# Performance work log

Measured on AMD Instinct MI355X. Metric: run time of the kernel, lower is better.

## Reference

```python
import jax, jax.numpy as jnp
import numpy as np

N, E, D = 50000, 800000, 64  # nodes, edges, hidden (in_hid == out_hid, n_heads == 1)


def setup_inputs() -> dict:
    key = jax.random.key(0)
    ks = jax.random.split(key, 12)

    def lin(k, out_d, in_d):
        k1, k2 = jax.random.split(k)
        s = 1.0 / np.sqrt(in_d)
        W = jax.random.uniform(k1, (out_d, in_d), minval=-s, maxval=s, dtype=jnp.float32)
        b = jax.random.uniform(k2, (out_d,), minval=-s, maxval=s, dtype=jnp.float32)
        return W, b

    Wt, bt = lin(ks[0], D, D + 1)   # w_transfer: Linear(d_input+1, d_k)
    Wq, bq = lin(ks[1], D, D)
    Wks, bks = lin(ks[2], D, D)
    Wkd, bkd = lin(ks[3], D, D)
    Wvs, bvs = lin(ks[4], D, D)
    Wvd, bvd = lin(ks[5], D, D)
    return {
        "x": jax.random.normal(ks[6], (N, D), dtype=jnp.float32),
        "edge_index": jax.random.randint(ks[7], (2, E), 0, N),
        "edge_time": jax.random.uniform(ks[8], (E,), dtype=jnp.float32),
        "x_time": jax.random.uniform(ks[9], (N,), dtype=jnp.float32),
        "edge_same": jax.random.randint(ks[10], (E,), 0, 2).astype(jnp.float32),
        "ln_gamma": jnp.ones((D,), jnp.float32),
        "ln_beta": jnp.zeros((D,), jnp.float32),
        "Wt": Wt, "bt": bt, "Wq": Wq, "bq": bq,
        "Wks": Wks, "bks": bks, "Wkd": Wkd, "bkd": bkd,
        "Wvs": Wvs, "bvs": bvs, "Wvd": Wvd, "bvd": bvd,
    }


def _gelu(x):
    return jax.nn.gelu(x, approximate=False)  # torch F.gelu default (erf)


def _temporal_enc(t):
    # TemporalEncoding: div_term[j] = 1/10000^(2*(j//2)/D); sin on even cols, cos on odd
    j = jnp.arange(D)
    div = 1.0 / jnp.power(jnp.float32(10000.0), (2.0 * (j // 2)).astype(jnp.float32) / D)
    pe = (t.reshape(-1, 1) * 200.0) * div[None, :]  # [E, D]
    return jnp.where((j % 2 == 0)[None, :], jnp.sin(pe), jnp.cos(pe))


def reference(x, edge_index, edge_time, x_time, edge_same, ln_gamma, ln_beta,
              Wt, bt, Wq, bq, Wks, bks, Wkd, bkd, Wvs, bvs, Wvd, bvd):
    residual = x
    # LayerNorm(d_input)
    mu = jnp.mean(x, axis=-1, keepdims=True)
    var = jnp.var(x, axis=-1, keepdims=True)
    xn = (x - mu) / jnp.sqrt(var + 1e-5) * ln_gamma + ln_beta

    src, dst = edge_index[0], edge_index[1]  # x_j = source, x_i = target (PyG default)
    x_j = xn[src]                            # [E, D] gather
    x_i = xn[dst]                            # [E, D] gather
    es = edge_same.reshape(-1, 1)            # [E, 1]

    te = _temporal_enc(edge_time)            # [E, D]
    xt = _gelu(jnp.concatenate([x_j, edge_time.reshape(-1, 1)], axis=1) @ Wt.T + bt) + te

    q = x_i @ Wq.T + bq
    k = es * (xt @ Wks.T + bks) + (1.0 - es) * (xt @ Wkd.T + bkd)
    att = jnp.sum(k * q, axis=-1) / jnp.sqrt(jnp.float32(D))  # [E]

    # PyG-style segment softmax over edges sharing the same receiver
    m = jax.ops.segment_max(att, dst, num_segments=N)
    m = jnp.where(jnp.isfinite(m), m, 0.0)
    ex = jnp.exp(att - m[dst])
    denom = jax.ops.segment_sum(ex, dst, num_segments=N)
    attn = ex / (denom[dst] + 1e-16)         # [E]

    v = es * (xt @ Wvs.T + bvs) + (1.0 - es) * (xt @ Wvd.T + bvd)
    aggr = jax.ops.segment_sum(attn[:, None] * v, dst, num_segments=N)  # [N, D]

    return residual + _gelu(aggr)            # dropout is identity in eval
```

## Files before the change

kernel.cpp:

```cpp
#include <hip/hip_runtime.h>
#include <hip/hip_bf16.h>
#include <math.h>

#define D 64

typedef __attribute__((ext_vector_type(8))) short bf16x8;
typedef __attribute__((ext_vector_type(8))) _Float16 f16x8;
typedef __attribute__((ext_vector_type(8))) unsigned short u16x8;
typedef __attribute__((ext_vector_type(4))) float f32x4;
typedef unsigned short u16;

__device__ __forceinline__ float gelu_erf(float x) {
    return 0.5f * x * (1.0f + erff(x * 0.70710678118654752f));
}
__device__ __forceinline__ float gelu_fast(float x) {
    float t = x * fmaf(x * x, -0.1029432f, -2.3022080f);
    float e = __builtin_amdgcn_exp2f(t);
    return x * __builtin_amdgcn_rcpf(1.0f + e);
}
__device__ __forceinline__ u16 f2bf(float v) {
    __hip_bfloat16 h = __float2bfloat16(v);
    return *(u16*)&h;
}
__device__ __forceinline__ float bf2f(u16 v) {
    return __uint_as_float(((unsigned int)v) << 16);
}
__device__ __forceinline__ u16 f2h(float v) {
    _Float16 h = (_Float16)v;
    return __builtin_bit_cast(u16, h);
}
__device__ __forceinline__ void atomic_pk_add_f16(u16* addr, float lo, float hi) {
    unsigned int p = (unsigned int)f2h(lo) | ((unsigned int)f2h(hi) << 16);
    asm volatile("global_atomic_pk_add_f16 %0, %1, off sc1" :: "v"(addr), "v"(p));
}
__device__ __forceinline__ int pi_perm(int p) { return ((p & 3) << 4) | (p >> 2); }

__device__ __forceinline__ float rowsum16(float v) {
    int x;
    x = __builtin_amdgcn_update_dpp(0, __builtin_bit_cast(int, v), 0xB1, 0xF, 0xF, true);
    v += __builtin_bit_cast(float, x);
    x = __builtin_amdgcn_update_dpp(0, __builtin_bit_cast(int, v), 0x4E, 0xF, 0xF, true);
    v += __builtin_bit_cast(float, x);
    x = __builtin_amdgcn_update_dpp(0, __builtin_bit_cast(int, v), 0x141, 0xF, 0xF, true);
    v += __builtin_bit_cast(float, x);
    x = __builtin_amdgcn_update_dpp(0, __builtin_bit_cast(int, v), 0x140, 0xF, 0xF, true);
    v += __builtin_bit_cast(float, x);
    return v;
}

__global__ __launch_bounds__(256) void prep_hist(
    const float* __restrict__ Wt, const float* __restrict__ Wq,
    const float* __restrict__ Wks, const float* __restrict__ Wkd,
    const float* __restrict__ Wvs, const float* __restrict__ Wvd,
    u16* __restrict__ WtB, u16* __restrict__ WqB,
    u16* __restrict__ WksB, u16* __restrict__ WkdB,
    u16* __restrict__ WvsB, u16* __restrict__ WvdB,
    const int* __restrict__ ei, const float* __restrict__ esame,
    int* __restrict__ cnt, int E)
{
    if (blockIdx.x < 12) {
        int task = blockIdx.x * 4 + (threadIdx.x >> 6);
        int lane = threadIdx.x & 63;
        int wsel = task >> 3, f = task & 7;
        int c = lane & 15, quad = lane >> 4;
        int nt = f >> 1, kk = f & 1;
        for (int j = 0; j < 8; ++j) {
            int n = nt * 16 + c, k = kk * 32 + quad * 8 + j;
            float v; u16* dp; bool h16 = false;
            switch (wsel) {
                case 0: v = Wt[n * 65 + k];  dp = WtB;  break;
                case 1: v = Wq[n * 64 + k];  dp = WqB;  break;
                case 2: v = Wks[k * 64 + n]; dp = WksB; break;
                case 3: v = Wkd[k * 64 + n]; dp = WkdB; break;
                case 4: v = Wvs[n * 64 + pi_perm(k)]; dp = WvsB; h16 = true; break;
                default: v = Wvd[n * 64 + pi_perm(k)]; dp = WvdB; h16 = true; break;
            }
            dp[(f * 64 + lane) * 8 + j] = h16 ? f2h(v) : f2bf(v);
        }
    } else {
        int gid = (blockIdx.x - 12) * 256 + threadIdx.x;
        int stride = (gridDim.x - 12) * 256;
        for (int e = gid; e < E; e += stride) {
            int key = 2 * ei[E + e] + (esame[e] > 0.5f ? 0 : 1);
            atomicAdd(&cnt[key], 1);
        }
    }
}

#define SCAN_CHUNK 2048

__global__ __launch_bounds__(256) void scan_phaseA(const int* __restrict__ cnt,
                                                   int* __restrict__ bsum, int M)
{
    int base = blockIdx.x * SCAN_CHUNK;
    int s = 0;
    for (int i = threadIdx.x; i < SCAN_CHUNK; i += 256) {
        int idx = base + i;
        s += (idx < M) ? cnt[idx] : 0;
    }
    #pragma unroll
    for (int o = 32; o; o >>= 1) s += __shfl_xor(s, o);
    __shared__ int red[4];
    if ((threadIdx.x & 63) == 0) red[threadIdx.x >> 6] = s;
    __syncthreads();
    if (threadIdx.x == 0) bsum[blockIdx.x] = red[0] + red[1] + red[2] + red[3];
}

__global__ __launch_bounds__(256) void scan_phaseC(const int* __restrict__ cnt,
                                                   const int* __restrict__ bsum,
                                                   int* __restrict__ cursor, int M)
{
    __shared__ int wsum[4];
    __shared__ int sboff;
    if (threadIdx.x < 64) {
        int v = ((int)threadIdx.x < (int)blockIdx.x) ? bsum[threadIdx.x] : 0;
        #pragma unroll
        for (int o = 32; o; o >>= 1) v += __shfl_xor(v, o);
        if (threadIdx.x == 0) sboff = v;
    }
    int base = blockIdx.x * SCAN_CHUNK;
    int i0 = base + threadIdx.x * 8;
    int vals[8];
    int tsum = 0;
    #pragma unroll
    for (int j = 0; j < 8; ++j) {
        int idx = i0 + j;
        vals[j] = (idx < M) ? cnt[idx] : 0;
        tsum += vals[j];
    }
    int lane = threadIdx.x & 63;
    int w = threadIdx.x >> 6;
    int inc = tsum;
    #pragma unroll
    for (int o = 1; o < 64; o <<= 1) {
        int v = __shfl_up(inc, o);
        if (lane >= o) inc += v;
    }
    if (lane == 63) wsum[w] = inc;
    __syncthreads();
    int woff = 0;
    #pragma unroll
    for (int k = 0; k < 4; ++k) woff += (k < w) ? wsum[k] : 0;
    int excl = woff + (inc - tsum) + sboff;
    #pragma unroll
    for (int j = 0; j < 8; ++j) {
        int idx = i0 + j;
        if (idx < M) cursor[idx] = excl;
        excl += vals[j];
    }
}

__global__ __launch_bounds__(256) void scatter_qgemm(
    const int* __restrict__ ei, const float* __restrict__ et,
    const float* __restrict__ esame, int* __restrict__ cursor,
    int4* __restrict__ evk, int E, int GS,
    const float* __restrict__ x, const float* __restrict__ gamma, const float* __restrict__ beta,
    const u16* __restrict__ WqB, const u16* __restrict__ WksB, const u16* __restrict__ WkdB,
    const float* __restrict__ bq, const float* __restrict__ bks, const float* __restrict__ bkd,
    u16* __restrict__ xnb, u16* __restrict__ qk2, float* __restrict__ bq2, int N)
{
    __shared__ u16 qtile[4][16 * 64];
    __shared__ u16 stile[4][32 * 64];

    if (blockIdx.x < GS) {
        int e = blockIdx.x * 256 + threadIdx.x;
        if (e < E) {
            int key = 2 * ei[E + e] + (esame[e] > 0.5f ? 0 : 1);
            int pos = atomicAdd(&cursor[key], 1);
            evk[pos] = make_int4(key, __float_as_int(et[e]), ei[e], 0);
        }
        return;
    }

    const int lane = threadIdx.x & 63;
    const int c = lane & 15, quad = lane >> 4;
    const int w = threadIdx.x >> 6;
    const int wave = (blockIdx.x - GS) * 4 + w;
    const int n0r = wave * 16;
    const bool active = n0r < N;
    const int n0 = active ? n0r : 0;
    const int rowA = (n0 + c < N) ? n0 + c : N - 1;

    const float* xrow = x + (long)rowA * D;
    f32x4 xa = *(const f32x4*)(xrow + quad * 8);
    f32x4 xb = *(const f32x4*)(xrow + quad * 8 + 4);
    f32x4 xc = *(const f32x4*)(xrow + 32 + quad * 8);
    f32x4 xd = *(const f32x4*)(xrow + 32 + quad * 8 + 4);
    float s = 0.f, s2 = 0.f;
    #pragma unroll
    for (int j = 0; j < 4; ++j) {
        s += xa[j] + xb[j] + xc[j] + xd[j];
        s2 += xa[j] * xa[j] + xb[j] * xb[j] + xc[j] * xc[j] + xd[j] * xd[j];
    }
    s += __shfl_xor(s, 16);  s += __shfl_xor(s, 32);
    s2 += __shfl_xor(s2, 16); s2 += __shfl_xor(s2, 32);
    float mu = s * (1.0f / 64.0f);
    float var = s2 * (1.0f / 64.0f) - mu * mu;
    float rinv = rsqrtf(var + 1e-5f);
    f32x4 ga = *(const f32x4*)(gamma + quad * 8);
    f32x4 gb = *(const f32x4*)(gamma + quad * 8 + 4);
    f32x4 gc = *(const f32x4*)(gamma + 32 + quad * 8);
    f32x4 gd = *(const f32x4*)(gamma + 32 + quad * 8 + 4);
    f32x4 ba = *(const f32x4*)(beta + quad * 8);
    f32x4 bb = *(const f32x4*)(beta + quad * 8 + 4);
    f32x4 bc = *(const f32x4*)(beta + 32 + quad * 8);
    f32x4 bd = *(const f32x4*)(beta + 32 + quad * 8 + 4);
    bf16x8 a0, a1;
    #pragma unroll
    for (int j = 0; j < 4; ++j) {
        a0[j]     = (short)f2bf(fmaf((xa[j] - mu) * rinv, ga[j], ba[j]));
        a0[4 + j] = (short)f2bf(fmaf((xb[j] - mu) * rinv, gb[j], bb[j]));
        a1[j]     = (short)f2bf(fmaf((xc[j] - mu) * rinv, gc[j], bc[j]));
        a1[4 + j] = (short)f2bf(fmaf((xd[j] - mu) * rinv, gd[j], bd[j]));
    }
    *(bf16x8*)(xnb + (long)rowA * D + quad * 8) = a0;
    *(bf16x8*)(xnb + (long)rowA * D + 32 + quad * 8) = a1;

    float bqc[4], bksc[4], bkdc[4];
    #pragma unroll
    for (int t = 0; t < 4; ++t) {
        bqc[t] = bq[t * 16 + c]; bksc[t] = bks[t * 16 + c]; bkdc[t] = bkd[t * 16 + c];
    }

    f32x4 accq[4];
    #pragma unroll
    for (int t = 0; t < 4; ++t) {
        bf16x8 b0 = *(const bf16x8*)(WqB + ((t * 2 + 0) * 64 + lane) * 8);
        bf16x8 b1 = *(const bf16x8*)(WqB + ((t * 2 + 1) * 64 + lane) * 8);
        f32x4 z = {0.f, 0.f, 0.f, 0.f};
        z = __builtin_amdgcn_mfma_f32_16x16x32_bf16(a0, b0, z, 0, 0, 0);
        z = __builtin_amdgcn_mfma_f32_16x16x32_bf16(a1, b1, z, 0, 0, 0);
        accq[t] = z;
    }
    #pragma unroll
    for (int r = 0; r < 4; ++r) {
        float qv[4], ss = 0.f, sd = 0.f;
        #pragma unroll
        for (int t = 0; t < 4; ++t) {
            qv[t] = accq[t][r] + bqc[t];
            ss = fmaf(qv[t], bksc[t], ss);
            sd = fmaf(qv[t], bkdc[t], sd);
        }
        #pragma unroll
        for (int o = 1; o < 16; o <<= 1) { ss += __shfl_xor(ss, o); sd += __shfl_xor(sd, o); }
        int nrow = n0 + quad * 4 + r;
        if (active && c == 0 && nrow < N)
            *(float2*)(bq2 + 2 * nrow) = make_float2(ss, sd);
        #pragma unroll
        for (int t = 0; t < 4; ++t)
            qtile[w][(quad * 4 + r) * 64 + t * 16 + c] = f2bf(qv[t]);
    }
    __syncthreads();

    const u16* qrow = &qtile[w][c * 64 + quad * 8];
    bf16x8 q0 = *(const bf16x8*)(qrow);
    bf16x8 q1 = *(const bf16x8*)(qrow + 32);
    #pragma unroll
    for (int t = 0; t < 4; ++t) {
        bf16x8 bs0 = *(const bf16x8*)(WksB + ((t * 2 + 0) * 64 + lane) * 8);
        bf16x8 bs1 = *(const bf16x8*)(WksB + ((t * 2 + 1) * 64 + lane) * 8);
        bf16x8 bd0 = *(const bf16x8*)(WkdB + ((t * 2 + 0) * 64 + lane) * 8);
        bf16x8 bd1 = *(const bf16x8*)(WkdB + ((t * 2 + 1) * 64 + lane) * 8);
        f32x4 zs = {0.f, 0.f, 0.f, 0.f}, zd = {0.f, 0.f, 0.f, 0.f};
        zs = __builtin_amdgcn_mfma_f32_16x16x32_bf16(q0, bs0, zs, 0, 0, 0);
        zs = __builtin_amdgcn_mfma_f32_16x16x32_bf16(q1, bs1, zs, 0, 0, 0);
        zd = __builtin_amdgcn_mfma_f32_16x16x32_bf16(q0, bd0, zd, 0, 0, 0);
        zd = __builtin_amdgcn_mfma_f32_16x16x32_bf16(q1, bd1, zd, 0, 0, 0);
        #pragma unroll
        for (int r = 0; r < 4; ++r) {
            int m = quad * 4 + r;
            stile[w][(2 * m + 0) * 64 + c * 4 + t] = f2bf(zs[r]);
            stile[w][(2 * m + 1) * 64 + c * 4 + t] = f2bf(zd[r]);
        }
    }
    __syncthreads();
    if (active) {
        int nrows = min(16, N - n0);
        const u16x8* sp = (const u16x8*)&stile[w][0];
        u16x8* dp = (u16x8*)(qk2 + (long)(2 * n0) * D);
        int cnt8 = nrows * 16;
        for (int j = lane; j < cnt8; j += 64) dp[j] = sp[j];
    }
}

template<bool FULL>
__device__ __forceinline__ void edge_run(
    const int4* __restrict__ evk, const u16* __restrict__ xnb,
    const bf16x8* bfrag, const float* btc, const float* w64c,
    const float* dvr, float phr,
    const u16* __restrict__ qk2, const float* __restrict__ bq2,
    u16* __restrict__ A, float* __restrict__ den,
    int base, int end, int qchunk, int c, int quad)
{
    int cur_key = -1;
    float racc0 = 0.f, racc1 = 0.f, racc2 = 0.f, racc3 = 0.f, rden = 0.f;
    float qf0 = 0.f, qf1 = 0.f, qf2 = 0.f, qf3 = 0.f, bqk = 0.f;

    const int rowbase = base + (c >> 2) * qchunk + (c & 3);
    const int qbase   = base + quad * qchunk;

    for (int i = 0; i < qchunk; i += 4) {
        int eidx = rowbase + i;
        int ec = FULL ? eidx : min(eidx, end - 1);
        int srcL = ((const int*)(evk + ec))[2];

        const u16* ar = xnb + srcL * D + quad * 8;
        bf16x8 a0 = *(const bf16x8*)(ar);
        bf16x8 a1 = *(const bf16x8*)(ar + 32);

        int qb = qbase + i;
        int2 kt0 = *(const int2*)(evk + (FULL ? qb     : min(qb,     end - 1)));
        int2 kt1 = *(const int2*)(evk + (FULL ? qb + 1 : min(qb + 1, end - 1)));
        int2 kt2 = *(const int2*)(evk + (FULL ? qb + 2 : min(qb + 2, end - 1)));
        int2 kt3 = *(const int2*)(evk + (FULL ? qb + 3 : min(qb + 3, end - 1)));

        f32x4 acc[4];
        #pragma unroll
        for (int t = 0; t < 4; ++t) {
            f32x4 z = {0.f, 0.f, 0.f, 0.f};
            z = __builtin_amdgcn_mfma_f32_16x16x32_bf16(a0, bfrag[t * 2 + 0], z, 0, 0, 0);
            z = __builtin_amdgcn_mfma_f32_16x16x32_bf16(a1, bfrag[t * 2 + 1], z, 0, 0, 0);
            acc[t] = z;
        }

        #pragma unroll
        for (int r = 0; r < 4; ++r) {
            int2 kt = (r == 0) ? kt0 : (r == 1) ? kt1 : (r == 2) ? kt2 : kt3;
            int keym = kt.x;
            float tm = __int_as_float(kt.y);

            float x0 = acc[0][r] + fmaf(tm, w64c[0], btc[0]);
            float x1 = acc[1][r] + fmaf(tm, w64c[1], btc[1]);
            float x2 = acc[2][r] + fmaf(tm, w64c[2], btc[2]);
            float x3 = acc[3][r] + fmaf(tm, w64c[3], btc[3]);
            float v0 = gelu_fast(x0) + __builtin_amdgcn_sinf(fmaf(tm, dvr[0], phr));
            float v1 = gelu_fast(x1) + __builtin_amdgcn_sinf(fmaf(tm, dvr[1], phr));
            float v2 = gelu_fast(x2) + __builtin_amdgcn_sinf(fmaf(tm, dvr[2], phr));
            float v3 = gelu_fast(x3) + __builtin_amdgcn_sinf(fmaf(tm, dvr[3], phr));

            if (keym != cur_key) {
                if (cur_key >= 0) {
                    u16* ap = A + cur_key * D + c * 4;
                    atomic_pk_add_f16(ap, racc0, racc1);
                    atomic_pk_add_f16(ap + 2, racc2, racc3);
                    if (c == 0) atomicAdd(&den[cur_key], rden);
                }
                cur_key = keym;
                ushort4 q4 = *(const ushort4*)(qk2 + cur_key * D + c * 4);
                qf0 = bf2f(q4.x); qf1 = bf2f(q4.y); qf2 = bf2f(q4.z); qf3 = bf2f(q4.w);
                bqk = bq2[cur_key] * 0.18033688011f;
                racc0 = racc1 = racc2 = racc3 = 0.f;
                rden = 0.f;
            }

            float p = v0 * qf0;
            p = fmaf(v1, qf1, p);
            p = fmaf(v2, qf2, p);
            p = fmaf(v3, qf3, p);
            p = rowsum16(p);

            float ex = __builtin_amdgcn_exp2f(fmaf(p, 0.18033688011f, bqk));
            if (!FULL && (qbase + i + r >= end)) ex = 0.f;

            racc0 = fmaf(ex, v0, racc0);
            racc1 = fmaf(ex, v1, racc1);
            racc2 = fmaf(ex, v2, racc2);
            racc3 = fmaf(ex, v3, racc3);
            rden += ex;
        }
    }

    if (cur_key >= 0) {
        u16* ap = A + cur_key * D + c * 4;
        atomic_pk_add_f16(ap, racc0, racc1);
        atomic_pk_add_f16(ap + 2, racc2, racc3);
        if (c == 0) atomicAdd(&den[cur_key], rden);
    }
}

__global__ __launch_bounds__(256) void edge_pass(
    const int4* __restrict__ evk, const u16* __restrict__ xnb, const u16* __restrict__ WtB,
    const float* __restrict__ Wt, const float* __restrict__ bt,
    const u16* __restrict__ qk2, const float* __restrict__ bq2,
    u16* __restrict__ A, float* __restrict__ den, int E, int chunk)
{
    const int lane = threadIdx.x & 63;
    const int c = lane & 15, quad = lane >> 4;
    const int wave = blockIdx.x * 4 + (threadIdx.x >> 6);
    const int base = wave * chunk;
    if (base >= E) return;
    const int end = min(base + chunk, E);
    const int qchunk = chunk >> 2;

    bf16x8 bfrag[8];
    #pragma unroll
    for (int f = 0; f < 8; ++f)
        bfrag[f] = *(const bf16x8*)(WtB + (f * 64 + lane) * 8);

    float btc[4], w64c[4], dvr[4];
    #pragma unroll
    for (int t = 0; t < 4; ++t) {
        int dim = t * 16 + c;
        btc[t] = bt[dim];
        w64c[t] = Wt[dim * 65 + 64];
        dvr[t] = 31.830988618f * expf(-9.210340371976184f * (float)(2 * (dim >> 1)) * (1.0f / 64.0f));
    }
    const float phr = (c & 1) ? 0.25f : 0.0f;

    if (base + chunk <= E)
        edge_run<true>(evk, xnb, bfrag, btc, w64c, dvr, phr, qk2, bq2, A, den,
                       base, end, qchunk, c, quad);
    else
        edge_run<false>(evk, xnb, bfrag, btc, w64c, dvr, phr, qk2, bq2, A, den,
                        base, end, qchunk, c, quad);
}

__global__ __launch_bounds__(256) void vgemm(
    const float* __restrict__ x, const u16* __restrict__ A, const float* __restrict__ den,
    const u16* __restrict__ WvsB, const u16* __restrict__ WvdB,
    const float* __restrict__ bvs, const float* __restrict__ bvd,
    float* __restrict__ out, int N)
{
    const int lane = threadIdx.x & 63;
    const int c = lane & 15, quad = lane >> 4;
    const int wave = blockIdx.x * 4 + (threadIdx.x >> 6);
    const int n0 = wave * 16;
    if (n0 >= N) return;
    const int rowA = (n0 + c < N) ? n0 + c : N - 1;

    float bvsc[4], bvdc[4];
    #pragma unroll
    for (int t = 0; t < 4; ++t) { bvsc[t] = bvs[t * 16 + c]; bvdc[t] = bvd[t * 16 + c]; }

    const u16* srow = A + (long)(2 * rowA) * D + quad * 8;
    const u16* drow = A + (long)(2 * rowA + 1) * D + quad * 8;
    f16x8 s0 = *(const f16x8*)(srow);
    f16x8 s1 = *(const f16x8*)(srow + 32);
    f16x8 d0 = *(const f16x8*)(drow);
    f16x8 d1 = *(const f16x8*)(drow + 32);

    f32x4 oacc[4];
    #pragma unroll
    for (int t = 0; t < 4; ++t) {
        f16x8 bs0 = *(const f16x8*)(WvsB + ((t * 2 + 0) * 64 + lane) * 8);
        f16x8 bs1 = *(const f16x8*)(WvsB + ((t * 2 + 1) * 64 + lane) * 8);
        f16x8 bd0 = *(const f16x8*)(WvdB + ((t * 2 + 0) * 64 + lane) * 8);
        f16x8 bd1 = *(const f16x8*)(WvdB + ((t * 2 + 1) * 64 + lane) * 8);
        f32x4 z = {0.f, 0.f, 0.f, 0.f};
        z = __builtin_amdgcn_mfma_f32_16x16x32_f16(s0, bs0, z, 0, 0, 0);
        z = __builtin_amdgcn_mfma_f32_16x16x32_f16(s1, bs1, z, 0, 0, 0);
        z = __builtin_amdgcn_mfma_f32_16x16x32_f16(d0, bd0, z, 0, 0, 0);
        z = __builtin_amdgcn_mfma_f32_16x16x32_f16(d1, bd1, z, 0, 0, 0);
        oacc[t] = z;
    }

    #pragma unroll
    for (int r = 0; r < 4; ++r) {
        int n = n0 + quad * 4 + r;
        if (n >= N) continue;
        float ds = den[2 * n], dd = den[2 * n + 1];
        float inv = 1.0f / (ds + dd + 1e-16f);
        float fs = ds * inv, fd = dd * inv;
        #pragma unroll
        for (int t = 0; t < 4; ++t) {
            long idx = (long)n * D + t * 16 + c;
            float o = fmaf(oacc[t][r], inv, fmaf(fs, bvsc[t], fd * bvdc[t]));
            out[idx] = x[idx] + gelu_erf(o);
        }
    }
}

extern "C" void kernel_launch(void* const* d_in, const int* in_sizes, int n_in,
                              void* d_out, int out_size, void* d_ws, size_t ws_size,
                              hipStream_t stream) {
    const float* x        = (const float*)d_in[0];
    const int*   ei       = (const int*)d_in[1];
    const float* et       = (const float*)d_in[2];
    const float* esame    = (const float*)d_in[4];
    const float* ln_gamma = (const float*)d_in[5];
    const float* ln_beta  = (const float*)d_in[6];
    const float* Wt  = (const float*)d_in[7];
    const float* bt  = (const float*)d_in[8];
    const float* Wq  = (const float*)d_in[9];
    const float* bq  = (const float*)d_in[10];
    const float* Wks = (const float*)d_in[11];
    const float* bks = (const float*)d_in[12];
    const float* Wkd = (const float*)d_in[13];
    const float* bkd = (const float*)d_in[14];
    const float* Wvs = (const float*)d_in[15];
    const float* bvs = (const float*)d_in[16];
    const float* Wvd = (const float*)d_in[17];
    const float* bvd = (const float*)d_in[18];
    float* out = (float*)d_out;

    const int N = in_sizes[0] / D;
    const int E = in_sizes[2];
    const int M = 2 * N;

    u16* A      = (u16*)d_ws;
    float* den  = (float*)(A + (long)M * D);
    int* cnt    = (int*)(den + M);
    int* cursor = cnt + M;
    float* bq2  = (float*)(cursor + M);
    int4* evk   = (int4*)(bq2 + M);
    int* bsum   = (int*)(evk + E);
    u16* xnb    = (u16*)(bsum + 256);
    u16* qk2    = xnb + (long)N * D;
    u16* WtB    = qk2 + (long)M * D;
    u16* WqB    = WtB + 4096;
    u16* WksB   = WqB + 4096;
    u16* WkdB   = WksB + 4096;
    u16* WvsB   = WkdB + 4096;
    u16* WvdB   = WvsB + 4096;

    hipMemsetAsync(A, 0, (size_t)M * D * 2 + (size_t)M * 4 * 2, stream);

    prep_hist<<<12 + 976, 256, 0, stream>>>(Wt, Wq, Wks, Wkd, Wvs, Wvd,
                                            WtB, WqB, WksB, WkdB, WvsB, WvdB,
                                            ei, esame, cnt, E);
    const int nbScan = (M + SCAN_CHUNK - 1) / SCAN_CHUNK;
    scan_phaseA<<<nbScan, 256, 0, stream>>>(cnt, bsum, M);
    scan_phaseC<<<nbScan, 256, 0, stream>>>(cnt, bsum, cursor, M);

    const int GS = (E + 255) / 256;
    const int GQ = ((N + 15) / 16 + 3) / 4;
    scatter_qgemm<<<GS + GQ, 256, 0, stream>>>(
        ei, et, esame, cursor, evk, E, GS,
        x, ln_gamma, ln_beta, WqB, WksB, WkdB, bq, bks, bkd,
        xnb, qk2, bq2, N);

    const int nwaves = 2048 * 4;
    const int chunk = ((E + nwaves * 16 - 1) / (nwaves * 16)) * 16;
    edge_pass<<<2048, 256, 0, stream>>>(evk, xnb, WtB, Wt, bt,
                                        qk2, bq2, A, den, E, chunk);
    vgemm<<<GQ, 256, 0, stream>>>(x, A, den, WvsB, WvdB, bvs, bvd, out, N);
}
```

Baseline: 268.6 us.

## Record per-edge rank in histogram to replace scatter atomics with plain offsets

```diff
diff --git a/kernel.cpp b/kernel.cpp
--- a/kernel.cpp
+++ b/kernel.cpp
@@ -56,7 +56,7 @@
     u16* __restrict__ WksB, u16* __restrict__ WkdB,
     u16* __restrict__ WvsB, u16* __restrict__ WvdB,
     const int* __restrict__ ei, const float* __restrict__ esame,
-    int* __restrict__ cnt, int E)
+    int* __restrict__ cnt, int* __restrict__ rank, int E)
 {
     if (blockIdx.x < 12) {
         int task = blockIdx.x * 4 + (threadIdx.x >> 6);
@@ -80,9 +80,21 @@
     } else {
         int gid = (blockIdx.x - 12) * 256 + threadIdx.x;
         int stride = (gridDim.x - 12) * 256;
-        for (int e = gid; e < E; e += stride) {
-            int key = 2 * ei[E + e] + (esame[e] > 0.5f ? 0 : 1);
-            atomicAdd(&cnt[key], 1);
+        int e[4]; bool v[4]; int key[4];
+        #pragma unroll
+        for (int j = 0; j < 4; ++j) { e[j] = gid + j * stride; v[j] = e[j] < E; }
+        #pragma unroll
+        for (int j = 0; j < 4; ++j) {
+            if (v[j]) key[j] = 2 * ei[E + e[j]] + (esame[e[j]] > 0.5f ? 0 : 1);
+        }
+        int r[4];
+        #pragma unroll
+        for (int j = 0; j < 4; ++j) {
+            if (v[j]) r[j] = atomicAdd(&cnt[key[j]], 1);
+        }
+        #pragma unroll
+        for (int j = 0; j < 4; ++j) {
+            if (v[j]) rank[e[j]] = r[j];
         }
     }
 }
@@ -152,7 +164,8 @@
 
 __global__ __launch_bounds__(256) void scatter_qgemm(
     const int* __restrict__ ei, const float* __restrict__ et,
-    const float* __restrict__ esame, int* __restrict__ cursor,
+    const float* __restrict__ esame, const int* __restrict__ cursor,
+    const int* __restrict__ rank,
     int4* __restrict__ evk, int E, int GS,
     const float* __restrict__ x, const float* __restrict__ gamma, const float* __restrict__ beta,
     const u16* __restrict__ WqB, const u16* __restrict__ WksB, const u16* __restrict__ WkdB,
@@ -163,11 +176,28 @@
     __shared__ u16 stile[4][32 * 64];
 
     if (blockIdx.x < GS) {
-        int e = blockIdx.x * 256 + threadIdx.x;
-        if (e < E) {
-            int key = 2 * ei[E + e] + (esame[e] > 0.5f ? 0 : 1);
-            int pos = atomicAdd(&cursor[key], 1);
-            evk[pos] = make_int4(key, __float_as_int(et[e]), ei[e], 0);
+        int gid = blockIdx.x * 256 + threadIdx.x;
+        int stride = GS * 256;
+        int e[4]; bool v[4]; int key[4]; int rk[4]; int src[4]; float tv[4];
+        #pragma unroll
+        for (int j = 0; j < 4; ++j) { e[j] = gid + j * stride; v[j] = e[j] < E; }
+        #pragma unroll
+        for (int j = 0; j < 4; ++j) {
+            if (v[j]) {
+                key[j] = 2 * ei[E + e[j]] + (esame[e[j]] > 0.5f ? 0 : 1);
+                rk[j] = rank[e[j]];
+                src[j] = ei[e[j]];
+                tv[j] = et[e[j]];
+            }
+        }
+        int pos[4];
+        #pragma unroll
+        for (int j = 0; j < 4; ++j) {
+            if (v[j]) pos[j] = cursor[key[j]] + rk[j];
+        }
+        #pragma unroll
+        for (int j = 0; j < 4; ++j) {
+            if (v[j]) evk[pos[j]] = make_int4(key[j], __float_as_int(tv[j]), src[j], 0);
         }
         return;
     }
@@ -512,22 +542,26 @@
     u16* WkdB   = WksB + 4096;
     u16* WvsB   = WkdB + 4096;
     u16* WvdB   = WvsB + 4096;
-
-    hipMemsetAsync(A, 0, (size_t)M * D * 2 + (size_t)M * 4 * 2, stream);
-
-    prep_hist<<<12 + 976, 256, 0, stream>>>(Wt, Wq, Wks, Wkd, Wvs, Wvd,
-                                            WtB, WqB, WksB, WkdB, WvsB, WvdB,
-                                            ei, esame, cnt, E);
+    int* rank   = (int*)A;
+
+    hipMemsetAsync(cnt, 0, (size_t)M * 4, stream);
+
+    const int GH = (E + 256 * 4 - 1) / (256 * 4);
+    prep_hist<<<12 + GH, 256, 0, stream>>>(Wt, Wq, Wks, Wkd, Wvs, Wvd,
+                                           WtB, WqB, WksB, WkdB, WvsB, WvdB,
+                                           ei, esame, cnt, rank, E);
     const int nbScan = (M + SCAN_CHUNK - 1) / SCAN_CHUNK;
     scan_phaseA<<<nbScan, 256, 0, stream>>>(cnt, bsum, M);
     scan_phaseC<<<nbScan, 256, 0, stream>>>(cnt, bsum, cursor, M);
 
-    const int GS = (E + 255) / 256;
+    const int GS = (E + 256 * 4 - 1) / (256 * 4);
     const int GQ = ((N + 15) / 16 + 3) / 4;
     scatter_qgemm<<<GS + GQ, 256, 0, stream>>>(
-        ei, et, esame, cursor, evk, E, GS,
+        ei, et, esame, cursor, rank, evk, E, GS,
         x, ln_gamma, ln_beta, WqB, WksB, WkdB, bq, bks, bkd,
         xnb, qk2, bq2, N);
+
+    hipMemsetAsync(A, 0, (size_t)M * D * 2 + (size_t)M * 4, stream);
 
     const int nwaves = 2048 * 4;
     const int chunk = ((E + nwaves * 16 - 1) / (nwaves * 16)) * 16;
```

New measurement: 233.5 us. -13.1%, faster.
